# Performance work log

Measured on AMD Instinct MI355X. Metric: run time of the kernel, lower is better.

Reference implementation:

```python
import jax, jax.numpy as jnp
import numpy as np

BN_EPS = 1e-3


def _bn(x, gamma, beta):
    # training-mode BatchNorm1d: per-call batch statistics (biased variance)
    m = jnp.mean(x, axis=0)
    v = jnp.mean(jnp.square(x - m), axis=0)
    return gamma * (x - m) * jax.lax.rsqrt(v + BN_EPS) + beta


def setup_inputs() -> dict:
    key = jax.random.key(0)
    ks = jax.random.split(key, 8)
    N, V, Cin, Cout = 1_000_000, 100_000, 16, 64
    return {
        "feat": jax.random.normal(ks[0], (V, Cin), dtype=jnp.float32),
        "points_xyz": jax.random.normal(ks[1], (N, Cin), dtype=jnp.float32),
        "unq_inv": jax.random.randint(ks[2], (N,), 0, V),
        "W_pre": jax.random.normal(ks[3], (Cin, Cout), dtype=jnp.float32) * (1.0 / np.sqrt(Cin)),
        "b_pre": jnp.zeros((Cout,), dtype=jnp.float32),
        "gamma_pre": jnp.ones((Cout,), dtype=jnp.float32),
        "beta_pre": jnp.zeros((Cout,), dtype=jnp.float32),
        "W_pos": jax.random.normal(ks[4], (Cout, Cout), dtype=jnp.float32) * (1.0 / np.sqrt(Cout)),
        "b_pos": jnp.zeros((Cout,), dtype=jnp.float32),
        "gamma_n": jnp.ones((Cout,), dtype=jnp.float32),
        "beta_n": jnp.zeros((Cout,), dtype=jnp.float32),
    }


def reference(feat, points_xyz, unq_inv, W_pre, b_pre, gamma_pre, beta_pre,
              W_pos, b_pos, gamma_n, beta_n):
    V = feat.shape[0]
    # per-point branch: pre_mix (Linear + BN), sin/cos gating, scatter-add to voxels
    p = _bn(points_xyz @ W_pre + b_pre, gamma_pre, beta_pre)      # [N, Cout]
    pw = p @ W_pos + b_pos                                        # [N, Cout]
    feat_add_sin = jax.ops.segment_sum(p * jnp.sin(pw), unq_inv, num_segments=V)  # [V, Cout]
    feat_add_cos = jax.ops.segment_sum(p * jnp.cos(pw), unq_inv, num_segments=V)
    # per-voxel (center) branch through the SAME pre_mix / pos_weight layers
    f = _bn(feat @ W_pre + b_pre, gamma_pre, beta_pre)            # [V, Cout]
    mw = f @ W_pos + b_pos
    center_sin = f * jnp.sin(mw)
    center_cos = f * jnp.cos(mw)
    final = (feat_add_sin + center_sin) * center_sin + (feat_add_cos + center_cos) * center_cos
    return jax.nn.relu(_bn(final, gamma_n, beta_n))
```

## Files before the change

### kernel.cpp

```cpp
#include <hip/hip_runtime.h>
#include <cstdint>
#include <cstddef>

constexpr int CIN  = 16;
constexpr int COUT = 64;
constexpr int NMOM = 16 + 136;
constexpr double BN_EPS = 1e-3;

typedef float v2f __attribute__((ext_vector_type(2)));
typedef __fp16 v2h __attribute__((ext_vector_type(2)));
constexpr float INV_2PI = 0.15915494309189535f;

constexpr int P_A = 0, P_B = 64, P_C = 128, P_WC = 192, P_SZ = 192 + CIN * COUT;

constexpr int CHUNK = 512;
constexpr int MB = 256;

__device__ __forceinline__ unsigned bc_u(v2h h) { return __builtin_bit_cast(unsigned, h); }
__device__ __forceinline__ v2h bc_h(unsigned u) { return __builtin_bit_cast(v2h, u); }

__global__ __launch_bounds__(256, 2) void moments2_kernel(const float* __restrict__ xyz, int n1,
                                                       const float* __restrict__ feat, int n2,
                                                       const int* __restrict__ unq,
                                                       int* __restrict__ cnt,
                                                       float* __restrict__ partP,
                                                       float* __restrict__ partF)
{
    const int bb  = blockIdx.x;
    const bool second = (bb >= MB);
    const float* x = second ? feat : xyz;
    const int    n = second ? n2 : n1;
    float* part    = second ? partF : partP;
    const int blk  = second ? bb - MB : bb;

    float acc[NMOM];
#pragma unroll
    for (int i = 0; i < NMOM; i++) acc[i] = 0.f;

    int tid = blk * 256 + threadIdx.x;
    int stride = MB * 256;
    for (int r = tid; r < n; r += stride) {
        const float4* xp = (const float4*)(x + (size_t)r * CIN);
        float4 a0 = xp[0], a1 = xp[1], a2 = xp[2], a3 = xp[3];
        if (!second) atomicAdd(cnt + unq[r], 1);
        float v[16] = {a0.x,a0.y,a0.z,a0.w, a1.x,a1.y,a1.z,a1.w,
                       a2.x,a2.y,a2.z,a2.w, a3.x,a3.y,a3.z,a3.w};
#pragma unroll
        for (int i = 0; i < 16; i++) acc[i] += v[i];
        int c = 16;
#pragma unroll
        for (int k = 0; k < 16; k++)
#pragma unroll
            for (int l = k; l < 16; l++) { acc[c] = fmaf(v[k], v[l], acc[c]); c++; }
    }

    const int lane = threadIdx.x & 63;
    const int wid  = threadIdx.x >> 6;
    float r0 = 0.f, r1 = 0.f, r2 = 0.f;
#pragma unroll
    for (int i = 0; i < NMOM; i++) {
        float s = acc[i];
#pragma unroll
        for (int off = 1; off < 64; off <<= 1) s += __shfl_xor(s, off, 64);
        if (i < 64)       { if (lane == i)       r0 = s; }
        else if (i < 128) { if (lane == i - 64)  r1 = s; }
        else              { if (lane == i - 128) r2 = s; }
    }

    __shared__ float red[4][NMOM];
    red[wid][lane] = r0;
    red[wid][64 + lane] = r1;
    if (lane < NMOM - 128) red[wid][128 + lane] = r2;
    __syncthreads();
    int t = threadIdx.x;
    if (t < NMOM) {
        float s = red[0][t] + red[1][t] + red[2][t] + red[3][t];
        part[(size_t)blk * NMOM + t] = s;
    }
}

__global__ __launch_bounds__(256) void prep_scanA(const float* __restrict__ Wpre, const float* __restrict__ bpre,
                            const float* __restrict__ gpre, const float* __restrict__ bepre,
                            const float* __restrict__ Wpos, const float* __restrict__ bpos,
                            const float* __restrict__ partP, const float* __restrict__ partF,
                            int nrows, int Np, int Vv,
                            float* __restrict__ prepP, float* __restrict__ prepF,
                            const int* __restrict__ cnt, int V,
                            int* __restrict__ chunkSum)
{
    const int t = threadIdx.x;
    const int lane = t & 63, wid = t >> 6;

    if (blockIdx.x >= 2) {
        const int b = blockIdx.x - 2;
        int base = b * CHUNK;
        int i0 = base + t * 2, i1 = i0 + 1;
        int s = ((i0 < V) ? cnt[i0] : 0) + ((i1 < V) ? cnt[i1] : 0);
        __shared__ int redc[4];
#pragma unroll
        for (int off = 1; off < 64; off <<= 1) s += __shfl_xor(s, off, 64);
        if (lane == 0) redc[wid] = s;
        __syncthreads();
        if (t == 0) chunkSum[b] = redc[0] + redc[1] + redc[2] + redc[3];
        return;
    }

    const int br = blockIdx.x;
    const float* part = br ? partF : partP;
    const double n    = br ? (double)Vv : (double)Np;
    const double inv_n = 1.0 / n;
    float* prep       = br ? prepF : prepP;

    __shared__ float sWpre[CIN * 64];
    __shared__ float sWpos[64 * 64];
    __shared__ double mom[NMOM];
    __shared__ double sS[64], sB[64];

    for (int i = t; i < CIN * 64; i += 256) sWpre[i] = Wpre[i];
    for (int i = t; i < 64 * 64; i += 256)  sWpos[i] = Wpos[i];

    if (t < NMOM) {
        double s0 = 0, s1 = 0, s2 = 0, s3 = 0, s4 = 0, s5 = 0, s6 = 0, s7 = 0;
        int r = 0;
        for (; r + 8 <= nrows; r += 8) {
            s0 += (double)part[(size_t)(r + 0) * NMOM + t];
            s1 += (double)part[(size_t)(r + 1) * NMOM + t];
            s2 += (double)part[(size_t)(r + 2) * NMOM + t];
            s3 += (double)part[(size_t)(r + 3) * NMOM + t];
            s4 += (double)part[(size_t)(r + 4) * NMOM + t];
            s5 += (double)part[(size_t)(r + 5) * NMOM + t];
            s6 += (double)part[(size_t)(r + 6) * NMOM + t];
            s7 += (double)part[(size_t)(r + 7) * NMOM + t];
        }
        for (; r < nrows; r++) s0 += (double)part[(size_t)r * NMOM + t];
        mom[t] = ((s0 + s1) + (s2 + s3)) + ((s4 + s5) + (s6 + s7));
    }
    __syncthreads();

    if (t < 64) {
        const int k = t;
        double mu[16];
#pragma unroll
        for (int i = 0; i < 16; i++) mu[i] = mom[i] * inv_n;
        double w[16];
#pragma unroll
        for (int i = 0; i < 16; i++) w[i] = (double)sWpre[i * 64 + k];

        double mk = (double)bpre[k];
#pragma unroll
        for (int i = 0; i < 16; i++) mk += mu[i] * w[i];

        double var = 0.0;
        int c = 16;
#pragma unroll
        for (int a = 0; a < 16; a++)
#pragma unroll
            for (int l = a; l < 16; l++) {
                double cov = mom[c] * inv_n - mu[a] * mu[l]; c++;
                var += (a == l ? 1.0 : 2.0) * w[a] * w[l] * cov;
            }

        double s_k = (double)gpre[k] / sqrt(var + BN_EPS);
        double B_k = (double)bepre[k] + s_k * ((double)bpre[k] - mk);
        sS[k] = s_k; sB[k] = B_k;
    }
    __syncthreads();

    if (t < 64) {
        const int k = t;
        double c0 = (double)bpos[k], c1 = 0.0;
        for (int j = 0; j < 64; j += 2) {
            c0 += sB[j]     * (double)sWpos[j * 64 + k];
            c1 += sB[j + 1] * (double)sWpos[(j + 1) * 64 + k];
        }
        prep[P_A + k] = (float)sS[k];
        prep[P_B + k] = (float)sB[k];
        prep[P_C + k] = (float)(c0 + c1);
    }

    {
        const int k  = t & 63;
        const int i0 = t >> 6;
        for (int i = i0; i < 16; i += 4) {
            double w0 = 0.0, w1 = 0.0;
            for (int j = 0; j < 64; j += 2) {
                w0 += (double)sWpre[i * 64 + j]     * sS[j]     * (double)sWpos[j * 64 + k];
                w1 += (double)sWpre[i * 64 + j + 1] * sS[j + 1] * (double)sWpos[(j + 1) * 64 + k];
            }
            prep[P_WC + i * 64 + k] = (float)(w0 + w1);
        }
    }
}

__global__ __launch_bounds__(64) void scanC(const int* __restrict__ cnt, int V, int N,
                                            const int* __restrict__ chunkSum,
                                            int* __restrict__ start,
                                            int* __restrict__ cursor)
{
    const int b = blockIdx.x;
    const int lane = threadIdx.x;

    int pv = 0;
    for (int i = lane; i < b; i += 64) pv += chunkSum[i];
#pragma unroll
    for (int off = 1; off < 64; off <<= 1) pv += __shfl_xor(pv, off, 64);
    const int chunkBase = pv;

    const int base = b * CHUNK + lane * 8;
    int e[8];
    int run = 0;
#pragma unroll
    for (int j = 0; j < 8; j++) {
        int idx = base + j;
        int c = (idx < V) ? cnt[idx] : 0;
        e[j] = run;
        run += c;
    }
    int incl = run;
#pragma unroll
    for (int off = 1; off < 64; off <<= 1) {
        int vv = __shfl_up(incl, off, 64);
        if (lane >= off) incl += vv;
    }
    int excl = incl - run;
    int myBase = chunkBase + excl;
#pragma unroll
    for (int j = 0; j < 8; j++) {
        int idx = base + j;
        if (idx < V) { start[idx] = myBase + e[j]; cursor[idx] = 0; }
    }
    if (b == 0 && lane == 0) start[V] = N;
}

__global__ __launch_bounds__(256) void scatter_kernel(const int* __restrict__ unq, int N,
                                                      const int* __restrict__ start,
                                                      int* __restrict__ cursor,
                                                      int* __restrict__ sortedIdx)
{
    int t = blockIdx.x * blockDim.x + threadIdx.x;
    int stride = gridDim.x * blockDim.x;
    for (; t < N; t += stride) {
        int v = unq[t];
        int pos = start[v] + atomicAdd(cursor + v, 1);
        sortedIdx[pos] = t;
    }
}

__global__ __launch_bounds__(256) void fused_pass(const float* __restrict__ xyz,
                                                  const float* __restrict__ feat,
                                                  const int* __restrict__ sortedIdx,
                                                  const int* __restrict__ start,
                                                  const float* __restrict__ Wpre,
                                                  const float* __restrict__ prepP,
                                                  const float* __restrict__ prepF,
                                                  float* __restrict__ outFinal,
                                                  float* __restrict__ statsPart, int V)
{
    const int lane = threadIdx.x & 63;
    const int wid  = threadIdx.x >> 6;
    const int rq   = lane >> 2;
    const int cc   = lane & 3;

    __shared__ uint2 ldsq[4][3][64];
    __shared__ unsigned sWcF2[8 * 64];
    uint2* bufA = ldsq[wid][0];
    uint2* bufB = ldsq[wid][1];
    uint2* remb = ldsq[wid][2];
    const int wslot = rq * 4 + cc;

    for (int i = threadIdx.x; i < 8 * 64; i += 256) {
        int fi = i >> 6, ch = i & 63;
        sWcF2[i] = bc_u(__builtin_amdgcn_cvt_pkrtz(prepF[P_WC + (2 * fi) * 64 + ch],
                                                   prepF[P_WC + (2 * fi + 1) * 64 + ch]));
    }
    __syncthreads();

    v2h wpre2[8], wcp2[8];
#pragma unroll
    for (int i = 0; i < 8; i++) {
        wpre2[i] = __builtin_amdgcn_cvt_pkrtz(Wpre[(2 * i) * 64 + lane],
                                              Wpre[(2 * i + 1) * 64 + lane]);
        wcp2[i]  = __builtin_amdgcn_cvt_pkrtz(prepP[P_WC + (2 * i) * 64 + lane],
                                              prepP[P_WC + (2 * i + 1) * 64 + lane]);
    }

    const float AP = prepP[P_A + lane], BP = prepP[P_B + lane];
    const float CPr = prepP[P_C + lane] * INV_2PI;
    const float AF = prepF[P_A + lane], BF = prepF[P_B + lane];
    const float CFr = prepF[P_C + lane] * INV_2PI;

    const int wave = __builtin_amdgcn_readfirstlane((int)((blockIdx.x * blockDim.x + threadIdx.x) >> 6));
    const int nw   = (gridDim.x * blockDim.x) >> 6;
    float s1 = 0.f, s2 = 0.f;

    auto prefetch = [&](int v, int& sb, int& m, uint2& u) {
        sb = __builtin_amdgcn_readfirstlane(start[v]);
        int se = __builtin_amdgcn_readfirstlane(start[v + 1]);
        m = se - sb;
        int ms0 = min(m, 15);
        int row = min(rq, ms0);
        int ridx = sortedIdx[sb + row];
        const float* bp = (row == ms0) ? (feat + (size_t)v * CIN)
                                       : (xyz  + (size_t)ridx * CIN);
        float4 q = *(const float4*)(bp + cc * 4);
        u.x = bc_u(__builtin_amdgcn_cvt_pkrtz(q.x, q.y));
        u.y = bc_u(__builtin_amdgcn_cvt_pkrtz(q.z, q.w));
    };

    auto pointmath = [&](const uint2* buf, int j, v2f& acc) {
        uint4 a = ((const uint4*)buf)[j * 2 + 0];
        uint4 b = ((const uint4*)buf)[j * 2 + 1];
        v2h xs[8] = {bc_h(a.x), bc_h(a.y), bc_h(a.z), bc_h(a.w),
                     bc_h(b.x), bc_h(b.y), bc_h(b.z), bc_h(b.w)};
        float dx = 0.f, dw = 0.f;
#pragma unroll
        for (int i = 0; i < 8; i++) {
            dx = __builtin_amdgcn_fdot2(xs[i], wpre2[i], dx, false);
            dw = __builtin_amdgcn_fdot2(xs[i], wcp2[i],  dw, false);
        }
        float p  = fmaf(AP, dx, BP);
        float r  = fmaf(dw, INV_2PI, CPr);
        float sv = __builtin_amdgcn_sinf(r);
        float cv = __builtin_amdgcn_cosf(r);
        acc += p * (v2f){sv, cv};
    };

    int v = wave;
    int sb = 0, m = 0;
    uint2* cur = bufA;
    uint2* nxt = bufB;
    if (v < V) {
        uint2 u; prefetch(v, sb, m, u);
        cur[wslot] = u;
    }

    while (v < V) {
        const int vn = v + nw;
        int sbn = 0, mn = 0; uint2 un = {};
        if (vn < V) prefetch(vn, sbn, mn, un);

        const int ms0 = min(m, 15);
        v2f acc = (v2f){0.f, 0.f};

        for (int j = 0; j < ms0; j++) pointmath(cur, j, acc);

        for (int base = 15; base < m; base += 16) {
            const int msr  = min(16, m - base);
            const int rowc = min(rq, msr - 1);
            int ridx = sortedIdx[sb + base + rowc];
            float4 q = *(const float4*)(xyz + (size_t)ridx * CIN + cc * 4);
            uint2 u;
            u.x = bc_u(__builtin_amdgcn_cvt_pkrtz(q.x, q.y));
            u.y = bc_u(__builtin_amdgcn_cvt_pkrtz(q.z, q.w));
            remb[wslot] = u;
            for (int j = 0; j < msr; j++) pointmath(remb, j, acc);
        }

        {
            uint4 a = ((const uint4*)cur)[ms0 * 2 + 0];
            uint4 b = ((const uint4*)cur)[ms0 * 2 + 1];
            v2h xs[8] = {bc_h(a.x), bc_h(a.y), bc_h(a.z), bc_h(a.w),
                         bc_h(b.x), bc_h(b.y), bc_h(b.z), bc_h(b.w)};
            float dx = 0.f, dw = 0.f;
#pragma unroll
            for (int i = 0; i < 8; i++) {
                dx = __builtin_amdgcn_fdot2(xs[i], wpre2[i], dx, false);
                dw = __builtin_amdgcn_fdot2(xs[i], bc_h(sWcF2[i * 64 + lane]), dw, false);
            }
            float f  = fmaf(AF, dx, BF);
            float r  = fmaf(dw, INV_2PI, CFr);
            float sv = __builtin_amdgcn_sinf(r);
            float cv = __builtin_amdgcn_cosf(r);
            float cs = f * sv, ccn = f * cv;
            float fin = fmaf(acc.x + cs, cs, (acc.y + ccn) * ccn);
            outFinal[(size_t)v * 64 + lane] = fin;
            s1 += fin;
            s2 = fmaf(fin, fin, s2);
        }

        if (vn < V) nxt[wslot] = un;
        uint2* tmp = cur; cur = nxt; nxt = tmp;
        v = vn; sb = sbn; m = mn;
    }

    __shared__ float sh1[4][64], sh2[4][64];
    sh1[wid][lane] = s1; sh2[wid][lane] = s2;
    __syncthreads();
    if (threadIdx.x < 64) {
        float t1 = sh1[0][lane] + sh1[1][lane] + sh1[2][lane] + sh1[3][lane];
        float t2 = sh2[0][lane] + sh2[1][lane] + sh2[2][lane] + sh2[3][lane];
        float* row = statsPart + (size_t)(blockIdx.x & 63) * 128;
        atomicAdd(row + lane, t1);
        atomicAdd(row + 64 + lane, t2);
    }
}

__global__ __launch_bounds__(256) void norm_kernel(float* __restrict__ out,
                                                   const float* __restrict__ sp,
                                                   const float* __restrict__ gn,
                                                   const float* __restrict__ bnb,
                                                   int V, size_t n4)
{
    __shared__ float sNs[64], sNb[64];
    const int t = threadIdx.x;
    if (t < 64) {
        double u1 = 0.0, u2 = 0.0;
#pragma unroll 4
        for (int r = 0; r < 64; r++) {
            u1 += (double)sp[(size_t)r * 128 + t];
            u2 += (double)sp[(size_t)r * 128 + 64 + t];
        }
        double mean = u1 / (double)V;
        double var  = u2 / (double)V - mean * mean;
        double ns   = (double)gn[t] / sqrt(var + BN_EPS);
        sNs[t] = (float)ns;
        sNb[t] = (float)((double)bnb[t] - ns * mean);
    }
    __syncthreads();

    const float4* ns4 = (const float4*)sNs;
    const float4* nb4 = (const float4*)sNb;
    float4* o4 = (float4*)out;
    size_t i = (size_t)blockIdx.x * blockDim.x + threadIdx.x;
    size_t stride = (size_t)gridDim.x * blockDim.x;
    for (; i < n4; i += stride) {
        int g = (int)(i & 15);
        float4 sc = ns4[g], bi = nb4[g];
        float4 w = o4[i];
        w.x = fmaxf(0.f, fmaf(sc.x, w.x, bi.x));
        w.y = fmaxf(0.f, fmaf(sc.y, w.y, bi.y));
        w.z = fmaxf(0.f, fmaf(sc.z, w.z, bi.z));
        w.w = fmaxf(0.f, fmaf(sc.w, w.w, bi.w));
        o4[i] = w;
    }
}

extern "C" void kernel_launch(void* const* d_in, const int* in_sizes, int n_in,
                              void* d_out, int out_size, void* d_ws, size_t ws_size,
                              hipStream_t stream)
{
    const float* feat  = (const float*)d_in[0];
    const float* xyz   = (const float*)d_in[1];
    const int*   unq   = (const int*)d_in[2];
    const float* Wpre  = (const float*)d_in[3];
    const float* bpre  = (const float*)d_in[4];
    const float* gpre  = (const float*)d_in[5];
    const float* bepre = (const float*)d_in[6];
    const float* Wpos  = (const float*)d_in[7];
    const float* bpos  = (const float*)d_in[8];
    const float* gn    = (const float*)d_in[9];
    const float* bnb   = (const float*)d_in[10];

    const int V = in_sizes[0] / CIN;
    const int N = in_sizes[1] / CIN;
    const int nch = (V + CHUNK - 1) / CHUNK;

    char* ws = (char*)d_ws;
    size_t off = 0;
    auto alloc = [&](size_t bytes) { void* p = ws + off; off += (bytes + 255) & ~size_t(255); return p; };

    int*   cnt       = (int*)alloc((size_t)V * 4);
    float* statsPart = (float*)alloc(64 * 128 * 4);
    const size_t zeroBytes = off;

    int*   cursor    = (int*)alloc((size_t)V * 4);
    int*   start     = (int*)alloc((size_t)(V + 1) * 4);
    int*   chunkSum  = (int*)alloc(256 * 4);
    int*   sortedIdx = (int*)alloc((size_t)(N + 64) * 4);

    float* partP = (float*)alloc((size_t)MB * NMOM * 4);
    float* partF = (float*)alloc((size_t)MB * NMOM * 4);
    float* prepP = (float*)alloc(P_SZ * 4);
    float* prepF = (float*)alloc(P_SZ * 4);

    hipMemsetAsync(d_ws, 0, zeroBytes, stream);

    moments2_kernel<<<2 * MB, 256, 0, stream>>>(xyz, N, feat, V, unq, cnt, partP, partF);
    prep_scanA<<<nch + 2, 256, 0, stream>>>(Wpre, bpre, gpre, bepre, Wpos, bpos,
                                            partP, partF, MB, N, V, prepP, prepF,
                                            cnt, V, chunkSum);
    scanC<<<nch, 64, 0, stream>>>(cnt, V, N, chunkSum, start, cursor);
    scatter_kernel<<<1024, 256, 0, stream>>>(unq, N, start, cursor, sortedIdx);
    fused_pass<<<2048, 256, 0, stream>>>(xyz, feat, sortedIdx, start, Wpre,
                                         prepP, prepF, (float*)d_out, statsPart, V);
    norm_kernel<<<512, 256, 0, stream>>>((float*)d_out, statsPart, gn, bnb, V,
                                         (size_t)out_size / 4);
}
```

Baseline: 222.3 us.

## Reuse histogram atomic return as slot index; scatter in four voxel-range passes

The counting atomic in the moments kernel now records its return value per point, so the scatter kernel no longer needs a second atomic cursor per voxel. The scatter is also split into four passes, each writing only points whose voxel falls in one quarter of the voxel range, to localize writes into sortedIdx. This removes N atomics and the cursor reset, but adds an N-sized slot array (extra write and read) and makes scatter read unq four times.

```diff
diff --git a/kernel.cpp b/kernel.cpp
--- a/kernel.cpp
+++ b/kernel.cpp
@@ -23,6 +23,7 @@
                                                        const float* __restrict__ feat, int n2,
                                                        const int* __restrict__ unq,
                                                        int* __restrict__ cnt,
+                                                       int* __restrict__ slot32,
                                                        float* __restrict__ partP,
                                                        float* __restrict__ partF)
 {
@@ -42,7 +43,7 @@
     for (int r = tid; r < n; r += stride) {
         const float4* xp = (const float4*)(x + (size_t)r * CIN);
         float4 a0 = xp[0], a1 = xp[1], a2 = xp[2], a3 = xp[3];
-        if (!second) atomicAdd(cnt + unq[r], 1);
+        if (!second) slot32[r] = atomicAdd(cnt + unq[r], 1);
         float v[16] = {a0.x,a0.y,a0.z,a0.w, a1.x,a1.y,a1.z,a1.w,
                        a2.x,a2.y,a2.z,a2.w, a3.x,a3.y,a3.z,a3.w};
 #pragma unroll
@@ -194,8 +195,7 @@
 
 __global__ __launch_bounds__(64) void scanC(const int* __restrict__ cnt, int V, int N,
                                             const int* __restrict__ chunkSum,
-                                            int* __restrict__ start,
-                                            int* __restrict__ cursor)
+                                            int* __restrict__ start)
 {
     const int b = blockIdx.x;
     const int lane = threadIdx.x;
@@ -227,22 +227,28 @@
 #pragma unroll
     for (int j = 0; j < 8; j++) {
         int idx = base + j;
-        if (idx < V) { start[idx] = myBase + e[j]; cursor[idx] = 0; }
+        if (idx < V) start[idx] = myBase + e[j];
     }
     if (b == 0 && lane == 0) start[V] = N;
 }
 
-__global__ __launch_bounds__(256) void scatter_kernel(const int* __restrict__ unq, int N,
+__global__ __launch_bounds__(256) void scatter_kernel(const int* __restrict__ unq,
+                                                      const int* __restrict__ slot32,
+                                                      int N, int V,
                                                       const int* __restrict__ start,
-                                                      int* __restrict__ cursor,
                                                       int* __restrict__ sortedIdx)
 {
-    int t = blockIdx.x * blockDim.x + threadIdx.x;
-    int stride = gridDim.x * blockDim.x;
-    for (; t < N; t += stride) {
-        int v = unq[t];
-        int pos = start[v] + atomicAdd(cursor + v, 1);
-        sortedIdx[pos] = t;
+    const int qsz = (V + 3) >> 2;
+    const int t0 = blockIdx.x * blockDim.x + threadIdx.x;
+    const int stride = gridDim.x * blockDim.x;
+    for (int k = 0; k < 4; k++) {
+        const int lo = k * qsz;
+        const int hi = min(lo + qsz, V);
+        for (int t = t0; t < N; t += stride) {
+            int v = unq[t];
+            if (v >= lo && v < hi)
+                sortedIdx[start[v] + slot32[t]] = t;
+        }
     }
 }
 
@@ -463,7 +469,7 @@
     float* statsPart = (float*)alloc(64 * 128 * 4);
     const size_t zeroBytes = off;
 
-    int*   cursor    = (int*)alloc((size_t)V * 4);
+    int*   slot32    = (int*)alloc((size_t)N * 4);
     int*   start     = (int*)alloc((size_t)(V + 1) * 4);
     int*   chunkSum  = (int*)alloc(256 * 4);
     int*   sortedIdx = (int*)alloc((size_t)(N + 64) * 4);
@@ -475,12 +481,12 @@
 
     hipMemsetAsync(d_ws, 0, zeroBytes, stream);
 
-    moments2_kernel<<<2 * MB, 256, 0, stream>>>(xyz, N, feat, V, unq, cnt, partP, partF);
+    moments2_kernel<<<2 * MB, 256, 0, stream>>>(xyz, N, feat, V, unq, cnt, slot32, partP, partF);
     prep_scanA<<<nch + 2, 256, 0, stream>>>(Wpre, bpre, gpre, bepre, Wpos, bpos,
                                             partP, partF, MB, N, V, prepP, prepF,
                                             cnt, V, chunkSum);
-    scanC<<<nch, 64, 0, stream>>>(cnt, V, N, chunkSum, start, cursor);
-    scatter_kernel<<<1024, 256, 0, stream>>>(unq, N, start, cursor, sortedIdx);
+    scanC<<<nch, 64, 0, stream>>>(cnt, V, N, chunkSum, start);
+    scatter_kernel<<<1024, 256, 0, stream>>>(unq, slot32, N, V, start, sortedIdx);
     fused_pass<<<2048, 256, 0, stream>>>(xyz, feat, sortedIdx, start, Wpre,
                                          prepP, prepF, (float*)d_out, statsPart, V);
     norm_kernel<<<512, 256, 0, stream>>>((float*)d_out, statsPart, gn, bnb, V,
```

New measurement: 187.8 us, median of 2. -15.5%, faster.
